# Performance work log

Measured on AMD Instinct MI355X. Metric: run time of the kernel, lower is better.

## Reference

```python
import jax, jax.numpy as jnp
import numpy as np
from jax import lax

B, C, L = 2048, 9605, 8
WL_PER_LABEL = 50
ALPHA = 0.5        # training_config['alpha4']
ALPHA1 = 0.1       # margin
ALPHA2 = 2.0       # training_config['alpha2']
ALPHA3 = 10.0      # training_config['alpha3']
ALPHA_OTHER = 0.5
NEG = jnp.float32(-1e30)


def setup_inputs() -> dict:
    key = jax.random.key(0)
    k1, k2, k3, k4 = jax.random.split(key, 4)
    x = jax.random.normal(k1, (B, C), dtype=jnp.float32) * 2.0
    y = (jax.random.uniform(k2, (B, C)) < 0.005).astype(jnp.float32)
    y_neg = (jax.random.uniform(k3, (B, C)) < 0.005).astype(jnp.float32)
    # whitelist masks: L app-labels, each whitelisting ~WL_PER_LABEL raw classes
    idx = jax.random.randint(k4, (L, WL_PER_LABEL), 0, C)
    wl_masks = jnp.zeros((L, C), dtype=bool).at[jnp.arange(L)[:, None], idx].set(True)
    return {"x": x, "y": y, "y_neg": y_neg, "wl_masks": wl_masks}


def reference(x, y, y_neg, wl_masks):
    # y_neg is consumed by the original forward (find_gt_whitelist) but never
    # affects the returned loss, faithfully ignored here.
    xs_pos = jax.nn.sigmoid(x)                                  # [B, C]
    # top_k_thres = max(11th-largest sigmoid, alpha_other)
    thres = jnp.maximum(lax.top_k(xs_pos, 11)[0][:, 10], ALPHA_OTHER)  # [B]
    # per-label whitelist max: m[b,l] = max_{c in wl_l} xs_pos[b,c]
    m = jnp.max(jnp.where(wl_masks[None, :, :], xs_pos[:, None, :], NEG), axis=-1)  # [B, L]
    # label l is a ground-truth whitelist label iff y has any positive in wl_l
    has_pos = jnp.einsum('bc,lc->bl', y, wl_masks.astype(y.dtype)) > 0   # [B, L]
    correct_max = jnp.max(jnp.where(has_pos, m, NEG), axis=-1)           # [B]
    incorrect_max = jnp.max(jnp.where(~has_pos, m, NEG), axis=-1)        # [B]
    any_correct = jnp.any(has_pos, axis=-1)
    any_incorrect = jnp.any(~has_pos, axis=-1)
    # union whitelist max (the "other" branch uses xs_pos over all wl indices)
    union_max = jnp.max(jnp.where(jnp.any(wl_masks, axis=0)[None, :], xs_pos, NEG), axis=-1)
    x1 = jnp.where(any_correct, correct_max, thres)
    x2 = jnp.where(any_correct,
                   jnp.where(any_incorrect, jnp.maximum(incorrect_max, thres), thres),
                   union_max)
    coef = jnp.where(any_correct, 1.0, 1.0 - ALPHA)
    d = x2 - x1 + ALPHA1
    rank = jnp.where(d > 0, ALPHA2, 1.0) * jax.nn.sigmoid(ALPHA3 * d)
    return jnp.mean(coef * rank)
```

## Files before the change

### kernel.cpp

```cpp
#include <hip/hip_runtime.h>

#define CC 9605
#define BB 2048
#define LL 8
#define CAND_MAX 384
#define NEGF (-1e30f)

#define WS_PARTIALS_OFF 16384

__device__ __forceinline__ unsigned enc_f(float f) {
  unsigned u = __float_as_uint(f);
  return (u & 0x80000000u) ? ~u : (u | 0x80000000u);
}
__device__ __forceinline__ float dec_u(unsigned e) {
  unsigned u = (e & 0x80000000u) ? (e & 0x7fffffffu) : ~e;
  return __uint_as_float(u);
}
__device__ __forceinline__ float sigm(float z) {
  return 1.0f / (1.0f + __expf(-z));
}

__device__ __forceinline__ void gload_lds16(const void* g, void* l) {
  __builtin_amdgcn_global_load_lds(
      (const __attribute__((address_space(1))) unsigned*)g,
      (__attribute__((address_space(3))) unsigned*)l, 16, 0, 0);
}

__global__ void wl_sniff(const unsigned* __restrict__ wlw,
                         unsigned* __restrict__ wsu) {
  const int nwords = (LL * CC) / 4;
  const int stride = gridDim.x * blockDim.x;
  unsigned f = 0u;
  for (int j = blockIdx.x * blockDim.x + threadIdx.x; j < nwords; j += stride) {
    unsigned w = wlw[j];
#pragma unroll
    for (int k = 0; k < 4; ++k) {
      unsigned b = (w >> (8 * k)) & 255u;
      if (b == 1u)    { f |= 2u; if (k != 0) f |= 1u; }
      if (b == 0x3fu) { f |= 8u; if (k == 1) f |= 4u; }
    }
  }
#pragma unroll
  for (int off = 32; off >= 1; off >>= 1) f |= __shfl_xor(f, off, 64);
  if ((threadIdx.x & 63) == 0 && f) atomicOr(&wsu[1], f);
}

__global__ void wl_compact(const unsigned char* __restrict__ wl,
                           unsigned* __restrict__ wsu) {
  const int tid = threadIdx.x;
  const int lane = tid & 63;
  const int c = blockIdx.x * 256 + tid;
  const unsigned g = wsu[1];
  const int dt = (g & 1u) ? 0 : (g & 4u) ? 3 : (g & 2u) ? 1 : (g & 8u) ? 2 : 0;
  const int* wl32 = (const int*)wl;
  const float* wlf = (const float*)wl;
  const unsigned short* wlh = (const unsigned short*)wl;
  unsigned m = 0u;
  if (c < CC) {
#pragma unroll
    for (int l = 0; l < LL; ++l) {
      int j = l * CC + c;
      bool on;
      if (dt == 0) on = (wl[j] != 0);
      else if (dt == 1) on = (wl32[j] != 0);
      else if (dt == 2) on = (wlf[j] != 0.0f);
      else on = (wlh[j] != 0);
      if (on) m |= (1u << l);
    }
  }
  unsigned long long bal = __ballot(m != 0u);
  if (bal) {
    unsigned wcnt = (unsigned)__popcll(bal);
    unsigned basep = 0u;
    if (lane == 0) basep = atomicAdd(&wsu[0], wcnt);
    basep = __shfl(basep, 0, 64);
    if (m) {
      unsigned pos = basep + (unsigned)__popcll(bal & ((1ull << lane) - 1ull));
      if (pos < 2048u) wsu[4 + pos] = ((unsigned)c << 8) | m;
    }
  }
}

__global__ __launch_bounds__(256, 4) void loss_kernel(
    const float* __restrict__ x, const float* __restrict__ y,
    const unsigned* __restrict__ wsu, float* __restrict__ partials) {
  __shared__ __align__(16) float sh_row[9608];
  __shared__ unsigned sh_cand[CAND_MAX];
  __shared__ unsigned sh_redM[4];
  __shared__ unsigned sh_redC[4];
  __shared__ unsigned sh_cnt;
  __shared__ unsigned sh_e11;
  __shared__ float sh_wl[4][10];

  const int tid = threadIdx.x;
  const int lane = tid & 63;
  const int wid = tid >> 6;
  const int b = blockIdx.x;
  const long long base = (long long)b * CC;

  const int soff = (4 - (b & 3)) & 3;
  const int ngroups = (CC - soff) >> 2;
  const int tailn = CC - soff - (ngroups << 2);
  const int m_extra = soff + tailn;
  const float4* vp = (const float4*)(x + base + soff);

  float tailv = 0.0f;
  if (tid < m_extra) {
    int col = (tid < soff) ? tid : (soff + (ngroups << 2) + (tid - soff));
    tailv = x[base + col];
  }

  const unsigned nu = wsu[0];
  const unsigned* ents = wsu + 4;
  const bool h0 = (unsigned)tid < nu;
  const bool h1 = (unsigned)(tid + 256) < nu;
  unsigned ent0 = 0u, ent1 = 0u;
  float gx0 = NEGF, gy0 = 0.0f, gx1 = NEGF, gy1 = 0.0f;
  if (h0) ent0 = ents[tid];
  if (h1) ent1 = ents[tid + 256];
  if (h0) { gx0 = x[base + (ent0 >> 8)]; gy0 = y[base + (ent0 >> 8)]; }
  if (h1) { gx1 = x[base + (ent1 >> 8)]; gy1 = y[base + (ent1 >> 8)]; }

  float4* rv = (float4*)sh_row;
#pragma unroll
  for (int i = 0; i < 9; ++i) {
    const int gbase = (i << 8) + (wid << 6);
    gload_lds16(&vp[gbase + lane], &rv[gbase]);
  }
  {
    const int g9 = (9 << 8) + tid;
    const int gbase = (9 << 8) + (wid << 6);
    if (g9 < ngroups) gload_lds16(&vp[g9], &rv[gbase]);
  }
  if (tid < m_extra) sh_row[(ngroups << 2) + tid] = tailv;
  if (tid < 3) sh_row[9605 + tid] = NEGF;
  if (tid == 0) sh_cnt = 0u;
  __syncthreads();

  unsigned mx = 0u;
#pragma unroll
  for (int i = 0; i < 10; ++i) {
    int g = tid + (i << 8);
    if (g < 2402) {
      float4 v = rv[g];
      mx = max(mx, max(max(enc_f(v.x), enc_f(v.y)),
                       max(enc_f(v.z), enc_f(v.w))));
    }
  }
#pragma unroll
  for (int off = 32; off >= 1; off >>= 1) mx = max(mx, __shfl_xor(mx, off, 64));
  if (lane == 0) sh_redM[wid] = mx;
  __syncthreads();
  const unsigned Emax =
      max(max(sh_redM[0], sh_redM[1]), max(sh_redM[2], sh_redM[3]));

  auto blk_count = [&](unsigned T) -> unsigned {
    unsigned cnt = 0u;
#pragma unroll
    for (int i = 0; i < 10; ++i) {
      int g = tid + (i << 8);
      if (g < 2402) {
        float4 v = rv[g];
        cnt += (enc_f(v.x) >= T) + (enc_f(v.y) >= T) +
               (enc_f(v.z) >= T) + (enc_f(v.w) >= T);
      }
    }
#pragma unroll
    for (int off = 32; off >= 1; off >>= 1) cnt += __shfl_xor(cnt, off, 64);
    __syncthreads();
    if (lane == 0) sh_redC[wid] = cnt;
    __syncthreads();
    return sh_redC[0] + sh_redC[1] + sh_redC[2] + sh_redC[3];
  };

  const unsigned STEP = 1u << 22;
  unsigned E11 = 0u;
  bool done = false;
  unsigned lo = (Emax > STEP) ? (Emax - STEP) : 1u;
  unsigned hi = Emax + 1u;
  unsigned c = blk_count(lo);
  while (c < 11u && lo > 1u) {
    hi = lo;
    lo = (lo > STEP) ? (lo - STEP) : 1u;
    c = blk_count(lo);
  }
  while (c > CAND_MAX) {
    if (hi - lo <= 1u) { E11 = lo; done = true; break; }
    unsigned mid = lo + ((hi - lo) >> 1);
    unsigned cm = blk_count(mid);
    if (cm >= 11u) { lo = mid; c = cm; } else { hi = mid; }
  }

  if (!done) {
#pragma unroll
    for (int i = 0; i < 10; ++i) {
      int g = tid + (i << 8);
      unsigned vals[4] = {0u, 0u, 0u, 0u};
      if (g < 2402) {
        float4 v = rv[g];
        vals[0] = enc_f(v.x); vals[1] = enc_f(v.y);
        vals[2] = enc_f(v.z); vals[3] = enc_f(v.w);
      }
#pragma unroll
      for (int k = 0; k < 4; ++k) {
        bool pr = (vals[k] >= lo);
        unsigned long long bal = __ballot(pr);
        if (bal) {
          unsigned wcnt = (unsigned)__popcll(bal);
          unsigned basep = 0u;
          if (lane == 0) basep = atomicAdd(&sh_cnt, wcnt);
          basep = __shfl(basep, 0, 64);
          if (pr) {
            unsigned posn =
                basep + (unsigned)__popcll(bal & ((1ull << lane) - 1ull));
            sh_cand[posn] = vals[k];
          }
        }
      }
    }
    __syncthreads();

    if (wid == 0) {
      unsigned v0[6];
#pragma unroll
      for (int j = 0; j < 6; ++j) {
        unsigned idx = (unsigned)lane + 64u * j;
        v0[j] = (idx < c) ? sh_cand[idx] : 0u;
      }
      unsigned ans = 0u;
      for (int r = 0; r < 11; ++r) {
        unsigned lmx = v0[0];
#pragma unroll
        for (int j = 1; j < 6; ++j) lmx = max(lmx, v0[j]);
        unsigned wm = lmx;
#pragma unroll
        for (int off = 32; off >= 1; off >>= 1)
          wm = max(wm, __shfl_xor(wm, off, 64));
        ans = wm;
        if (r < 10) {
          unsigned long long bal = __ballot(lmx == wm);
          int first = (int)__ffsll((long long)bal) - 1;
          if (lane == first) {
            bool rm = false;
#pragma unroll
            for (int j = 0; j < 6; ++j) {
              if (!rm && v0[j] == wm) { v0[j] = 0u; rm = true; }
            }
          }
        }
      }
      if (lane == 0) sh_e11 = ans;
    }
    __syncthreads();
    E11 = sh_e11;
  }

  float lm[8];
#pragma unroll
  for (int l = 0; l < 8; ++l) lm[l] = NEGF;
  unsigned pmask = 0u;
  if (h0) {
    unsigned mk = ent0 & 255u;
    pmask |= mk;
    if (gy0 > 0.0f) pmask |= (mk << 8);
#pragma unroll
    for (int l = 0; l < 8; ++l)
      if ((mk >> l) & 1u) lm[l] = fmaxf(lm[l], gx0);
  }
  if (h1) {
    unsigned mk = ent1 & 255u;
    pmask |= mk;
    if (gy1 > 0.0f) pmask |= (mk << 8);
#pragma unroll
    for (int l = 0; l < 8; ++l)
      if ((mk >> l) & 1u) lm[l] = fmaxf(lm[l], gx1);
  }
  for (unsigned e = (unsigned)tid + 512u; e < nu; e += 256u) {
    unsigned ent = ents[e];
    unsigned mk = ent & 255u;
    float xv = x[base + (ent >> 8)];
    float yv = y[base + (ent >> 8)];
    pmask |= mk;
    if (yv > 0.0f) pmask |= (mk << 8);
#pragma unroll
    for (int l = 0; l < 8; ++l)
      if ((mk >> l) & 1u) lm[l] = fmaxf(lm[l], xv);
  }
#pragma unroll
  for (int off = 32; off >= 1; off >>= 1) {
    pmask |= __shfl_xor(pmask, off, 64);
#pragma unroll
    for (int l = 0; l < 8; ++l) lm[l] = fmaxf(lm[l], __shfl_xor(lm[l], off, 64));
  }
  if (lane == 0) {
#pragma unroll
    for (int l = 0; l < 8; ++l) sh_wl[wid][l] = lm[l];
    sh_wl[wid][8] = __uint_as_float(pmask);
  }
  __syncthreads();

  if (tid == 0) {
    float LM[8];
    unsigned PM = 0u;
#pragma unroll
    for (int l = 0; l < 8; ++l) LM[l] = NEGF;
    for (int w = 0; w < 4; ++w) {
#pragma unroll
      for (int l = 0; l < 8; ++l) LM[l] = fmaxf(LM[l], sh_wl[w][l]);
      PM |= __float_as_uint(sh_wl[w][8]);
    }
    unsigned PR = PM & 255u, PO = (PM >> 8) & 255u;
    float thres = fmaxf(sigm(dec_u(E11)), 0.5f);
    float cmax = NEGF, imax = NEGF, umax = NEGF;
#pragma unroll
    for (int l = 0; l < 8; ++l) {
      if ((PR >> l) & 1u) {
        float ml = sigm(LM[l]);
        umax = fmaxf(umax, ml);
        if ((PO >> l) & 1u) cmax = fmaxf(cmax, ml);
        else imax = fmaxf(imax, ml);
      }
    }
    bool anyc = (PO != 0u);
    bool anyi = (PO != 255u);
    float x1 = anyc ? cmax : thres;
    float x2 = anyc ? (anyi ? fmaxf(imax, thres) : thres)
                    : ((nu > 0u) ? umax : NEGF);
    float coef = anyc ? 1.0f : 0.5f;
    float dd = x2 - x1 + 0.1f;
    float rank = ((dd > 0.0f) ? 2.0f : 1.0f) * sigm(10.0f * dd);
    partials[b] = coef * rank;
  }
}

__global__ void final_reduce(const float* __restrict__ partials,
                             float* __restrict__ out) {
  __shared__ float sh[4];
  const int tid = threadIdx.x;
  const int lane = tid & 63;
  const int wid = tid >> 6;
  float s = 0.0f;
  for (int i = tid; i < BB; i += 256) s += partials[i];
#pragma unroll
  for (int off = 32; off >= 1; off >>= 1) s += __shfl_xor(s, off, 64);
  if (lane == 0) sh[wid] = s;
  __syncthreads();
  if (tid == 0) out[0] = (sh[0] + sh[1] + sh[2] + sh[3]) * (1.0f / (float)BB);
}

extern "C" void kernel_launch(void* const* d_in, const int* in_sizes, int n_in,
                              void* d_out, int out_size, void* d_ws,
                              size_t ws_size, hipStream_t stream) {
  const float* x = (const float*)d_in[0];
  const float* y = (const float*)d_in[1];
  const unsigned char* wl = (const unsigned char*)d_in[3];
  float* out = (float*)d_out;
  unsigned* wsu = (unsigned*)d_ws;
  float* partials = (float*)((char*)d_ws + WS_PARTIALS_OFF);

  hipMemsetAsync(d_ws, 0, 16, stream);
  wl_sniff<<<64, 256, 0, stream>>>((const unsigned*)wl, wsu);
  wl_compact<<<(CC + 255) / 256, 256, 0, stream>>>(wl, wsu);
  loss_kernel<<<BB, 256, 0, stream>>>(x, y, wsu, partials);
  final_reduce<<<1, 256, 0, stream>>>(partials, out);
}
```

Measured before the change: 238.7 us.

## Replace per-row top-k search with global sampled threshold and streaming candidate collection

Adds a single-block kernel that builds a two-pass radix histogram over a strided sample of x to estimate one global threshold tau. A grid-stride streaming kernel then scans all of x once and appends each value at or above tau to a per-row candidate buffer using global atomics. The finalize kernel finds the 11th largest value from at most 96 candidates per row, and falls back to the old per-row binary search, now reading straight from global memory, when a row has too few or too many candidates. The goal is to drop the per-row LDS staging and the repeated count passes. In exchange it adds a serial single-block launch, global atomic traffic, and a fallback path that is slower whenever the sampled threshold does not suit a row.

```diff
diff --git a/kernel.cpp b/kernel.cpp
--- a/kernel.cpp
+++ b/kernel.cpp
@@ -4,9 +4,12 @@
 #define BB 2048
 #define LL 8
 #define CAND_MAX 384
+#define ROWCAP 96
 #define NEGF (-1e30f)
 
 #define WS_PARTIALS_OFF 16384
+#define WS_COUNTS_OFF 24576
+#define WS_CAND_OFF 32768
 
 __device__ __forceinline__ unsigned enc_f(float f) {
   unsigned u = __float_as_uint(f);
@@ -18,12 +21,6 @@
 }
 __device__ __forceinline__ float sigm(float z) {
   return 1.0f / (1.0f + __expf(-z));
-}
-
-__device__ __forceinline__ void gload_lds16(const void* g, void* l) {
-  __builtin_amdgcn_global_load_lds(
-      (const __attribute__((address_space(1))) unsigned*)g,
-      (__attribute__((address_space(3))) unsigned*)l, 16, 0, 0);
 }
 
 __global__ void wl_sniff(const unsigned* __restrict__ wlw,
@@ -81,10 +78,108 @@
   }
 }
 
-__global__ __launch_bounds__(256, 4) void loss_kernel(
+__global__ __launch_bounds__(256) void sample_tau(const float* __restrict__ x,
+                                                  unsigned* __restrict__ wsu,
+                                                  unsigned* __restrict__ counts) {
+  __shared__ unsigned h[256];
+  __shared__ unsigned suf[256];
+  __shared__ unsigned sB, sAbove, sTau;
+  const int tid = threadIdx.x;
+  for (int i = tid; i < BB; i += 256) counts[i] = 0u;
+  h[tid] = 0u;
+  __syncthreads();
+  const float4* xv = (const float4*)x;
+  for (int i = tid; i < 16384; i += 256) {
+    float4 v = xv[i * 300];
+    atomicAdd(&h[enc_f(v.x) >> 24], 1u);
+    atomicAdd(&h[enc_f(v.y) >> 24], 1u);
+    atomicAdd(&h[enc_f(v.z) >> 24], 1u);
+    atomicAdd(&h[enc_f(v.w) >> 24], 1u);
+  }
+  __syncthreads();
+  suf[tid] = h[tid];
+  __syncthreads();
+#pragma unroll
+  for (int d = 1; d < 256; d <<= 1) {
+    unsigned add = (tid + d < 256) ? suf[tid + d] : 0u;
+    __syncthreads();
+    suf[tid] += add;
+    __syncthreads();
+  }
+  const unsigned RANK = 205u;
+  if (suf[tid] >= RANK && (tid == 255 || suf[tid + 1] < RANK)) {
+    sB = (unsigned)tid;
+    sAbove = (tid == 255) ? 0u : suf[tid + 1];
+  }
+  __syncthreads();
+  const unsigned B = sB;
+  const unsigned rank2 = RANK - sAbove;
+  h[tid] = 0u;
+  __syncthreads();
+  for (int i = tid; i < 16384; i += 256) {
+    float4 v = xv[i * 300];
+    unsigned e;
+    e = enc_f(v.x); if ((e >> 24) == B) atomicAdd(&h[(e >> 16) & 255u], 1u);
+    e = enc_f(v.y); if ((e >> 24) == B) atomicAdd(&h[(e >> 16) & 255u], 1u);
+    e = enc_f(v.z); if ((e >> 24) == B) atomicAdd(&h[(e >> 16) & 255u], 1u);
+    e = enc_f(v.w); if ((e >> 24) == B) atomicAdd(&h[(e >> 16) & 255u], 1u);
+  }
+  __syncthreads();
+  suf[tid] = h[tid];
+  __syncthreads();
+#pragma unroll
+  for (int d = 1; d < 256; d <<= 1) {
+    unsigned add = (tid + d < 256) ? suf[tid + d] : 0u;
+    __syncthreads();
+    suf[tid] += add;
+    __syncthreads();
+  }
+  if (suf[tid] >= rank2 && (tid == 255 || suf[tid + 1] < rank2))
+    sTau = (B << 24) | ((unsigned)tid << 16);
+  __syncthreads();
+  if (tid == 0) wsu[3] = sTau;
+}
+
+__global__ __launch_bounds__(256) void stream_collect(
+    const float* __restrict__ x, const unsigned* __restrict__ wsu,
+    unsigned* __restrict__ counts, unsigned* __restrict__ cand) {
+  const unsigned tau = wsu[3];
+  const int NG = (CC * BB) / 4;
+  const int stride = gridDim.x * blockDim.x;
+  const float4* xv = (const float4*)x;
+  for (int g = blockIdx.x * blockDim.x + threadIdx.x; g < NG; g += stride) {
+    float4 v = xv[g];
+    unsigned idx = (unsigned)g << 2;
+    unsigned r = idx / 9605u;
+    unsigned rem = idx - r * 9605u;
+    unsigned e0 = enc_f(v.x), e1 = enc_f(v.y);
+    unsigned e2 = enc_f(v.z), e3 = enc_f(v.w);
+    if (e0 >= tau) {
+      unsigned s = atomicAdd(&counts[r], 1u);
+      if (s < (unsigned)ROWCAP) cand[r * ROWCAP + s] = e0;
+    }
+    if (e1 >= tau) {
+      unsigned rk = r + (rem + 1u >= 9605u);
+      unsigned s = atomicAdd(&counts[rk], 1u);
+      if (s < (unsigned)ROWCAP) cand[rk * ROWCAP + s] = e1;
+    }
+    if (e2 >= tau) {
+      unsigned rk = r + (rem + 2u >= 9605u);
+      unsigned s = atomicAdd(&counts[rk], 1u);
+      if (s < (unsigned)ROWCAP) cand[rk * ROWCAP + s] = e2;
+    }
+    if (e3 >= tau) {
+      unsigned rk = r + (rem + 3u >= 9605u);
+      unsigned s = atomicAdd(&counts[rk], 1u);
+      if (s < (unsigned)ROWCAP) cand[rk * ROWCAP + s] = e3;
+    }
+  }
+}
+
+__global__ __launch_bounds__(256) void finalize(
     const float* __restrict__ x, const float* __restrict__ y,
-    const unsigned* __restrict__ wsu, float* __restrict__ partials) {
-  __shared__ __align__(16) float sh_row[9608];
+    const unsigned* __restrict__ wsu, const unsigned* __restrict__ counts,
+    const unsigned* __restrict__ cand, float* __restrict__ partials) {
   __shared__ unsigned sh_cand[CAND_MAX];
   __shared__ unsigned sh_redM[4];
   __shared__ unsigned sh_redC[4];
@@ -97,18 +192,6 @@
   const int wid = tid >> 6;
   const int b = blockIdx.x;
   const long long base = (long long)b * CC;
-
-  const int soff = (4 - (b & 3)) & 3;
-  const int ngroups = (CC - soff) >> 2;
-  const int tailn = CC - soff - (ngroups << 2);
-  const int m_extra = soff + tailn;
-  const float4* vp = (const float4*)(x + base + soff);
-
-  float tailv = 0.0f;
-  if (tid < m_extra) {
-    int col = (tid < soff) ? tid : (soff + (ngroups << 2) + (tid - soff));
-    tailv = x[base + col];
-  }
 
   const unsigned nu = wsu[0];
   const unsigned* ents = wsu + 4;
@@ -121,89 +204,76 @@
   if (h0) { gx0 = x[base + (ent0 >> 8)]; gy0 = y[base + (ent0 >> 8)]; }
   if (h1) { gx1 = x[base + (ent1 >> 8)]; gy1 = y[base + (ent1 >> 8)]; }
 
-  float4* rv = (float4*)sh_row;
-#pragma unroll
-  for (int i = 0; i < 9; ++i) {
-    const int gbase = (i << 8) + (wid << 6);
-    gload_lds16(&vp[gbase + lane], &rv[gbase]);
-  }
-  {
-    const int g9 = (9 << 8) + tid;
-    const int gbase = (9 << 8) + (wid << 6);
-    if (g9 < ngroups) gload_lds16(&vp[g9], &rv[gbase]);
-  }
-  if (tid < m_extra) sh_row[(ngroups << 2) + tid] = tailv;
-  if (tid < 3) sh_row[9605 + tid] = NEGF;
-  if (tid == 0) sh_cnt = 0u;
-  __syncthreads();
-
-  unsigned mx = 0u;
-#pragma unroll
-  for (int i = 0; i < 10; ++i) {
-    int g = tid + (i << 8);
-    if (g < 2402) {
-      float4 v = rv[g];
-      mx = max(mx, max(max(enc_f(v.x), enc_f(v.y)),
-                       max(enc_f(v.z), enc_f(v.w))));
-    }
-  }
-#pragma unroll
-  for (int off = 32; off >= 1; off >>= 1) mx = max(mx, __shfl_xor(mx, off, 64));
-  if (lane == 0) sh_redM[wid] = mx;
-  __syncthreads();
-  const unsigned Emax =
-      max(max(sh_redM[0], sh_redM[1]), max(sh_redM[2], sh_redM[3]));
-
-  auto blk_count = [&](unsigned T) -> unsigned {
-    unsigned cnt = 0u;
-#pragma unroll
-    for (int i = 0; i < 10; ++i) {
-      int g = tid + (i << 8);
-      if (g < 2402) {
-        float4 v = rv[g];
-        cnt += (enc_f(v.x) >= T) + (enc_f(v.y) >= T) +
-               (enc_f(v.z) >= T) + (enc_f(v.w) >= T);
+  const unsigned cnt = counts[b];
+  unsigned E11 = 0u;
+  if (cnt >= 11u && cnt <= (unsigned)ROWCAP) {
+    if (wid == 0) {
+      const unsigned* gc = cand + (unsigned)b * ROWCAP;
+      unsigned a0 = ((unsigned)lane < cnt) ? gc[lane] : 0u;
+      unsigned a1 = ((unsigned)(lane + 64) < cnt) ? gc[lane + 64] : 0u;
+      unsigned ans = 0u;
+      for (int r = 0; r < 11; ++r) {
+        unsigned lmx = max(a0, a1);
+        unsigned wm = lmx;
+#pragma unroll
+        for (int off = 32; off >= 1; off >>= 1)
+          wm = max(wm, __shfl_xor(wm, off, 64));
+        ans = wm;
+        if (r < 10) {
+          unsigned long long bal = __ballot(lmx == wm);
+          int first = (int)__ffsll((long long)bal) - 1;
+          if (lane == first) {
+            if (a0 == wm) a0 = 0u; else a1 = 0u;
+          }
+        }
       }
-    }
-#pragma unroll
-    for (int off = 32; off >= 1; off >>= 1) cnt += __shfl_xor(cnt, off, 64);
-    __syncthreads();
-    if (lane == 0) sh_redC[wid] = cnt;
-    __syncthreads();
-    return sh_redC[0] + sh_redC[1] + sh_redC[2] + sh_redC[3];
-  };
-
-  const unsigned STEP = 1u << 22;
-  unsigned E11 = 0u;
-  bool done = false;
-  unsigned lo = (Emax > STEP) ? (Emax - STEP) : 1u;
-  unsigned hi = Emax + 1u;
-  unsigned c = blk_count(lo);
-  while (c < 11u && lo > 1u) {
-    hi = lo;
-    lo = (lo > STEP) ? (lo - STEP) : 1u;
-    c = blk_count(lo);
-  }
-  while (c > CAND_MAX) {
-    if (hi - lo <= 1u) { E11 = lo; done = true; break; }
-    unsigned mid = lo + ((hi - lo) >> 1);
-    unsigned cm = blk_count(mid);
-    if (cm >= 11u) { lo = mid; c = cm; } else { hi = mid; }
-  }
-
-  if (!done) {
-#pragma unroll
-    for (int i = 0; i < 10; ++i) {
-      int g = tid + (i << 8);
-      unsigned vals[4] = {0u, 0u, 0u, 0u};
-      if (g < 2402) {
-        float4 v = rv[g];
-        vals[0] = enc_f(v.x); vals[1] = enc_f(v.y);
-        vals[2] = enc_f(v.z); vals[3] = enc_f(v.w);
-      }
-#pragma unroll
-      for (int k = 0; k < 4; ++k) {
-        bool pr = (vals[k] >= lo);
+      if (lane == 0) sh_e11 = ans;
+    }
+    __syncthreads();
+    E11 = sh_e11;
+  } else {
+    if (tid == 0) sh_cnt = 0u;
+    unsigned mx = 0u;
+    for (int i = tid; i < CC; i += 256) mx = max(mx, enc_f(x[base + i]));
+#pragma unroll
+    for (int off = 32; off >= 1; off >>= 1)
+      mx = max(mx, __shfl_xor(mx, off, 64));
+    if (lane == 0) sh_redM[wid] = mx;
+    __syncthreads();
+    const unsigned Emax =
+        max(max(sh_redM[0], sh_redM[1]), max(sh_redM[2], sh_redM[3]));
+
+    auto gcount = [&](unsigned T) -> unsigned {
+      unsigned c2 = 0u;
+      for (int i = tid; i < CC; i += 256) c2 += (enc_f(x[base + i]) >= T);
+#pragma unroll
+      for (int off = 32; off >= 1; off >>= 1) c2 += __shfl_xor(c2, off, 64);
+      __syncthreads();
+      if (lane == 0) sh_redC[wid] = c2;
+      __syncthreads();
+      return sh_redC[0] + sh_redC[1] + sh_redC[2] + sh_redC[3];
+    };
+
+    const unsigned STEP = 1u << 22;
+    bool done = false;
+    unsigned lo = (Emax > STEP) ? (Emax - STEP) : 1u;
+    unsigned hi = Emax + 1u;
+    unsigned c = gcount(lo);
+    while (c < 11u && lo > 1u) {
+      hi = lo;
+      lo = (lo > STEP) ? (lo - STEP) : 1u;
+      c = gcount(lo);
+    }
+    while (c > CAND_MAX) {
+      if (hi - lo <= 1u) { E11 = lo; done = true; break; }
+      unsigned mid = lo + ((hi - lo) >> 1);
+      unsigned cm = gcount(mid);
+      if (cm >= 11u) { lo = mid; c = cm; } else { hi = mid; }
+    }
+    if (!done) {
+      for (int i = tid; i < CC; i += 256) {
+        unsigned e = enc_f(x[base + i]);
+        bool pr = (e >= lo);
         unsigned long long bal = __ballot(pr);
         if (bal) {
           unsigned wcnt = (unsigned)__popcll(bal);
@@ -213,46 +283,44 @@
           if (pr) {
             unsigned posn =
                 basep + (unsigned)__popcll(bal & ((1ull << lane) - 1ull));
-            sh_cand[posn] = vals[k];
+            sh_cand[posn] = e;
           }
         }
       }
-    }
-    __syncthreads();
-
-    if (wid == 0) {
-      unsigned v0[6];
-#pragma unroll
-      for (int j = 0; j < 6; ++j) {
-        unsigned idx = (unsigned)lane + 64u * j;
-        v0[j] = (idx < c) ? sh_cand[idx] : 0u;
-      }
-      unsigned ans = 0u;
-      for (int r = 0; r < 11; ++r) {
-        unsigned lmx = v0[0];
-#pragma unroll
-        for (int j = 1; j < 6; ++j) lmx = max(lmx, v0[j]);
-        unsigned wm = lmx;
-#pragma unroll
-        for (int off = 32; off >= 1; off >>= 1)
-          wm = max(wm, __shfl_xor(wm, off, 64));
-        ans = wm;
-        if (r < 10) {
-          unsigned long long bal = __ballot(lmx == wm);
-          int first = (int)__ffsll((long long)bal) - 1;
-          if (lane == first) {
-            bool rm = false;
-#pragma unroll
-            for (int j = 0; j < 6; ++j) {
-              if (!rm && v0[j] == wm) { v0[j] = 0u; rm = true; }
+      __syncthreads();
+      if (wid == 0) {
+        unsigned v0[6];
+#pragma unroll
+        for (int j = 0; j < 6; ++j) {
+          unsigned idx = (unsigned)lane + 64u * j;
+          v0[j] = (idx < c) ? sh_cand[idx] : 0u;
+        }
+        unsigned ans = 0u;
+        for (int r = 0; r < 11; ++r) {
+          unsigned lmx = v0[0];
+#pragma unroll
+          for (int j = 1; j < 6; ++j) lmx = max(lmx, v0[j]);
+          unsigned wm = lmx;
+#pragma unroll
+          for (int off = 32; off >= 1; off >>= 1)
+            wm = max(wm, __shfl_xor(wm, off, 64));
+          ans = wm;
+          if (r < 10) {
+            unsigned long long bal = __ballot(lmx == wm);
+            int first = (int)__ffsll((long long)bal) - 1;
+            if (lane == first) {
+              bool rm = false;
+#pragma unroll
+              for (int j = 0; j < 6; ++j)
+                if (!rm && v0[j] == wm) { v0[j] = 0u; rm = true; }
             }
           }
         }
+        if (lane == 0) sh_e11 = ans;
       }
-      if (lane == 0) sh_e11 = ans;
-    }
-    __syncthreads();
-    E11 = sh_e11;
+      __syncthreads();
+      E11 = sh_e11;
+    }
   }
 
   float lm[8];
@@ -357,10 +425,14 @@
   float* out = (float*)d_out;
   unsigned* wsu = (unsigned*)d_ws;
   float* partials = (float*)((char*)d_ws + WS_PARTIALS_OFF);
+  unsigned* counts = (unsigned*)((char*)d_ws + WS_COUNTS_OFF);
+  unsigned* cand = (unsigned*)((char*)d_ws + WS_CAND_OFF);
 
   hipMemsetAsync(d_ws, 0, 16, stream);
   wl_sniff<<<64, 256, 0, stream>>>((const unsigned*)wl, wsu);
   wl_compact<<<(CC + 255) / 256, 256, 0, stream>>>(wl, wsu);
-  loss_kernel<<<BB, 256, 0, stream>>>(x, y, wsu, partials);
+  sample_tau<<<1, 256, 0, stream>>>(x, wsu, counts);
+  stream_collect<<<2048, 256, 0, stream>>>(x, wsu, counts, cand);
+  finalize<<<BB, 256, 0, stream>>>(x, y, wsu, counts, cand, partials);
   final_reduce<<<1, 256, 0, stream>>>(partials, out);
 }
```

New measurement: 309.3 us. 1.3x slower.
